# Optimization experiments

Measured on AMD Instinct MI355X. Metric: run time of the kernel, lower is better.

The kernel has to match this reference:

```python
import jax, jax.numpy as jnp
import numpy as np

N = 200000       # nodes
E = 6400000      # edges
F_IN, H1, H2, C = 7, 32, 16, 2


def gcn_conv(x, W, b, src, dst, n):
    """PyG GCNConv: add self-loops, symmetric normalization, linear, scatter-add."""
    loop = jnp.arange(n, dtype=src.dtype)
    s = jnp.concatenate([src, loop])
    d = jnp.concatenate([dst, loop])
    # degree of target nodes (with self-loops)
    deg = jax.ops.segment_sum(jnp.ones_like(d, dtype=x.dtype), d, num_segments=n)
    dinv = jnp.where(deg > 0, jax.lax.rsqrt(deg), 0.0)
    h = x @ W                                  # [n, out]
    norm = dinv[s] * dinv[d]                   # [e+n]
    msg = h[s] * norm[:, None]                 # gather + normalize
    out = jax.ops.segment_sum(msg, d, num_segments=n)  # scatter-add aggregation
    return out + b


def setup_inputs() -> dict:
    key = jax.random.key(0)
    ks = jax.random.split(key, 8)
    x = jax.random.normal(ks[0], (N, F_IN), dtype=jnp.float32)
    edge_index = jax.random.randint(ks[1], (2, E), 0, N, dtype=jnp.int64)
    def glorot(k, fan_in, fan_out):
        lim = np.sqrt(6.0 / (fan_in + fan_out)).astype(np.float32)
        return jax.random.uniform(k, (fan_in, fan_out), jnp.float32, -lim, lim)
    return {
        "x": x,
        "edge_index": edge_index,
        "W1": glorot(ks[2], F_IN, H1), "b1": jnp.zeros((H1,), jnp.float32),
        "W2": glorot(ks[3], H1, H2), "b2": jnp.zeros((H2,), jnp.float32),
        "Wfc": glorot(ks[4], H2, C), "bfc": jnp.zeros((C,), jnp.float32),
    }


def reference(x, edge_index, W1, b1, W2, b2, Wfc, bfc):
    src, dst = edge_index[0], edge_index[1]
    h = jax.nn.relu(gcn_conv(x, W1, b1, src, dst, N))
    h = jax.nn.relu(gcn_conv(h, W2, b2, src, dst, N))
    return h @ Wfc + bfc
```

## Files before the change

kernel.cpp:

```cpp
#include <hip/hip_runtime.h>

#define NNODES 200000
#define NEDGES 6400000
#define FIN 7
#define FH1 32
#define FH2 16
#define NC 2

#define WB 128
#define WB_SHIFT 7
#define NBUCK ((NNODES + WB - 1) / WB)
#define NBLK 1024
#define CHUNK (NEDGES / NBLK)
#define EPT ((CHUNK + 255) / 256)
#define PSHIFT 18
#define SRCMASK ((1u << PSHIFT) - 1)

#define RSTRIDE 4608
#define BPT ((RSTRIDE + 255) / 256)
#define SCAP 5120


__global__ __launch_bounds__(256) void zero_cnt(int* __restrict__ cnt) {
    int i = blockIdx.x * 256 + threadIdx.x;
    if (i < NBUCK) cnt[i] = 0;
}


__global__ __launch_bounds__(256) void p2_sortres(const int* __restrict__ ei,
                                                  int* __restrict__ bucket_cur,
                                                  unsigned int* __restrict__ recs) {
    __shared__ int sorted[CHUNK];
    __shared__ int lcur[NBUCK];
    __shared__ int gbase[NBUCK];
    __shared__ int sm[256];
    int t = threadIdx.x;
    int blk = blockIdx.x;

    for (int i = t; i < NBUCK; i += 256) lcur[i] = 0;
    __syncthreads();

    int ebase = blk * CHUNK;
    int es[EPT];
    int rb[EPT];
#pragma unroll
    for (int j = 0; j < EPT; ++j) {
        int idx = j * 256 + t;
        if (idx < CHUNK) {
            int e = ebase + idx;
            int src = ei[e];
            int d = ei[NEDGES + e];
            int b = d >> WB_SHIFT;
            int rank = atomicAdd(&lcur[b], 1);
            es[j] = (int)((unsigned)src | ((unsigned)(d & (WB - 1)) << PSHIFT));
            rb[j] = (b << 16) | rank;
        }
    }
    __syncthreads();

    int base7 = t * 7;
    int loc[7];
    int s = 0;
#pragma unroll
    for (int k = 0; k < 7; ++k) {
        int idx = base7 + k;
        int v = (idx < NBUCK) ? lcur[idx] : 0;
        loc[k] = v;
        s += v;
    }
    sm[t] = s;
    __syncthreads();
    for (int off = 1; off < 256; off <<= 1) {
        int v = (t >= off) ? sm[t - off] : 0;
        __syncthreads();
        sm[t] += v;
        __syncthreads();
    }
    int run = sm[t] - s;
#pragma unroll
    for (int k = 0; k < 7; ++k) {
        int idx = base7 + k;
        if (idx < NBUCK) {
            lcur[idx] = run;
            if (loc[k] > 0)
                gbase[idx] = idx * RSTRIDE + atomicAdd(&bucket_cur[idx], loc[k]);
            run += loc[k];
        }
    }
    __syncthreads();

#pragma unroll
    for (int j = 0; j < EPT; ++j) {
        int idx = j * 256 + t;
        if (idx < CHUNK) {
            int b = rb[j] >> 16;
            int rank = rb[j] & 0xffff;
            sorted[lcur[b] + rank] = es[j];
        }
    }
    __syncthreads();

    for (int i = t; i < CHUNK; i += 256) {
        int lo = 0, hi = NBUCK - 1;
        while (lo < hi) {
            int mid = (lo + hi + 1) >> 1;
            if (lcur[mid] <= i) lo = mid; else hi = mid - 1;
        }
        int b = lo;
        recs[(size_t)gbase[b] + (i - lcur[b])] = (unsigned)sorted[i];
    }
}


__global__ __launch_bounds__(256) void p2b_sort(unsigned int* __restrict__ recs,
                                                const int* __restrict__ bucket_cur,
                                                const float* __restrict__ x,
                                                int* __restrict__ node_off,
                                                float4* __restrict__ gx) {
    __shared__ int sorted[SCAP];
    __shared__ int hist[WB], st[WB];
    int t = threadIdx.x;
    int b = blockIdx.x;
    if (t < WB) hist[t] = 0;
    __syncthreads();

    int beg = b * RSTRIDE;
    int cnt = bucket_cur[b];

    int es[BPT];
    int rr[BPT];
#pragma unroll
    for (int j = 0; j < BPT; ++j) {
        int i = j * 256 + t;
        if (i < cnt) {
            unsigned r = recs[(size_t)beg + i];
            int dl = r >> PSHIFT;
            int rank = atomicAdd(&hist[dl], 1);
            es[j] = (int)(r & SRCMASK);
            rr[j] = dl | (rank << 7);
        }
    }
    __syncthreads();

    if (t < WB) st[t] = hist[t];
    __syncthreads();
    for (int off = 1; off < WB; off <<= 1) {
        int v = 0;
        if (t < WB && t >= off) v = st[t - off];
        __syncthreads();
        if (t < WB) st[t] += v;
        __syncthreads();
    }
    if (t < WB) st[t] -= hist[t];
    __syncthreads();

#pragma unroll
    for (int j = 0; j < BPT; ++j) {
        int i = j * 256 + t;
        if (i < cnt) {
            int dl = rr[j] & (WB - 1);
            int rank = rr[j] >> 7;
            sorted[st[dl] + rank] = es[j];
        }
    }
    __syncthreads();

    for (int i = t; i < cnt; i += 256)
        recs[(size_t)beg + i] = (unsigned)sorted[i];

    int node = b * WB + t;
    if (t < WB && node < NNODES) {
        node_off[node] = beg + st[t];
        float di = rsqrtf((float)(1 + hist[t]));
        const float* xr = x + (size_t)node * FIN;
        float4 v0, v1;
        v0.x = xr[0] * di; v0.y = xr[1] * di; v0.z = xr[2] * di; v0.w = xr[3] * di;
        v1.x = xr[4] * di; v1.y = xr[5] * di; v1.z = xr[6] * di; v1.w = 0.0f;
        gx[(size_t)node * 2 + 0] = v0;
        gx[(size_t)node * 2 + 1] = v1;
    }
}


__global__ __launch_bounds__(256) void l1_fast(const unsigned int* __restrict__ recs,
                                               const int* __restrict__ node_off,
                                               const int* __restrict__ bucket_cur,
                                               const float4* __restrict__ gx,
                                               const float* __restrict__ W1,
                                               const float* __restrict__ b1,
                                               const float* __restrict__ W2,
                                               float4* __restrict__ y) {
    __shared__ int sl_src[SCAP];
    __shared__ int noffs[WB + 1];
    __shared__ float acc[WB][9];
    __shared__ float sW1[FIN * FH1];
    __shared__ float sb1[FH1];
    __shared__ float sW2[FH1 * FH2];
    int t = threadIdx.x;
    for (int i = t; i < FIN * FH1; i += 256) sW1[i] = W1[i];
    if (t < FH1) sb1[t] = b1[t];
    for (int i = t; i < FH1 * FH2; i += 256) sW2[i] = W2[i];

    int b = blockIdx.x;
    int beg = b * RSTRIDE;
    int cnt_all = bucket_cur[b];
    for (int i = t; i < WB; i += 256) {
        int idx = b * WB + i;
        noffs[i] = (idx < NNODES) ? node_off[idx] : beg + cnt_all;
    }
    if (t == 0) noffs[WB] = beg + cnt_all;
    __syncthreads();

    for (int i = t; i < cnt_all; i += 256) sl_src[i] = (int)recs[(size_t)beg + i];
    __syncthreads();

    int n = t >> 1;
    int hq = t & 1;
    int base = noffs[n] - beg;
    int cnt = noffs[n + 1] - noffs[n];
    float ax = 0.0f, ay = 0.0f, az = 0.0f, aw = 0.0f;
    int k = 0;
    for (; k + 7 < cnt; k += 8) {
        int s0 = sl_src[base + k];
        int s1 = sl_src[base + k + 1];
        int s2 = sl_src[base + k + 2];
        int s3 = sl_src[base + k + 3];
        int s4 = sl_src[base + k + 4];
        int s5 = sl_src[base + k + 5];
        int s6 = sl_src[base + k + 6];
        int s7 = sl_src[base + k + 7];
        float4 v0 = gx[(size_t)s0 * 2 + hq];
        float4 v1 = gx[(size_t)s1 * 2 + hq];
        float4 v2 = gx[(size_t)s2 * 2 + hq];
        float4 v3 = gx[(size_t)s3 * 2 + hq];
        float4 v4 = gx[(size_t)s4 * 2 + hq];
        float4 v5 = gx[(size_t)s5 * 2 + hq];
        float4 v6 = gx[(size_t)s6 * 2 + hq];
        float4 v7 = gx[(size_t)s7 * 2 + hq];
        ax += v0.x + v1.x; ay += v0.y + v1.y;
        az += v0.z + v1.z; aw += v0.w + v1.w;
        ax += v2.x + v3.x; ay += v2.y + v3.y;
        az += v2.z + v3.z; aw += v2.w + v3.w;
        ax += v4.x + v5.x; ay += v4.y + v5.y;
        az += v4.z + v5.z; aw += v4.w + v5.w;
        ax += v6.x + v7.x; ay += v6.y + v7.y;
        az += v6.z + v7.z; aw += v6.w + v7.w;
    }
    for (; k < cnt; ++k) {
        int s0 = sl_src[base + k];
        float4 v0 = gx[(size_t)s0 * 2 + hq];
        ax += v0.x; ay += v0.y; az += v0.z; aw += v0.w;
    }
    int kb = hq * 4;
    acc[n][kb + 0] = ax; acc[n][kb + 1] = ay;
    acc[n][kb + 2] = az; acc[n][kb + 3] = aw;
    __syncthreads();

    int node = b * WB + t;
    if (t >= WB || node >= NNODES) return;

    float di = rsqrtf((float)(1 + (noffs[t + 1] - noffs[t])));
    float4 g0 = gx[(size_t)node * 2], g1 = gx[(size_t)node * 2 + 1];
    float xa[FIN];
    xa[0] = (acc[t][0] + g0.x) * di;
    xa[1] = (acc[t][1] + g0.y) * di;
    xa[2] = (acc[t][2] + g0.z) * di;
    xa[3] = (acc[t][3] + g0.w) * di;
    xa[4] = (acc[t][4] + g1.x) * di;
    xa[5] = (acc[t][5] + g1.y) * di;
    xa[6] = (acc[t][6] + g1.z) * di;

    float h1[FH1];
#pragma unroll
    for (int j = 0; j < FH1; ++j) h1[j] = sb1[j];
#pragma unroll
    for (int f = 0; f < FIN; ++f) {
        float xv = xa[f];
#pragma unroll
        for (int j = 0; j < FH1; ++j) h1[j] = fmaf(xv, sW1[f * FH1 + j], h1[j]);
    }
#pragma unroll
    for (int j = 0; j < FH1; ++j) h1[j] = fmaxf(h1[j], 0.0f);

    float yv[FH2];
#pragma unroll
    for (int j = 0; j < FH2; ++j) yv[j] = 0.0f;
#pragma unroll
    for (int k2 = 0; k2 < FH1; ++k2) {
        float hv = h1[k2];
#pragma unroll
        for (int j = 0; j < FH2; ++j) yv[j] = fmaf(hv, sW2[k2 * FH2 + j], yv[j]);
    }

    size_t yb = (size_t)node * 4;
    float4 o;
    o.x = yv[0] * di; o.y = yv[1] * di; o.z = yv[2] * di; o.w = yv[3] * di;
    y[yb + 0] = o;
    o.x = yv[4] * di; o.y = yv[5] * di; o.z = yv[6] * di; o.w = yv[7] * di;
    y[yb + 1] = o;
    o.x = yv[8] * di; o.y = yv[9] * di; o.z = yv[10] * di; o.w = yv[11] * di;
    y[yb + 2] = o;
    o.x = yv[12] * di; o.y = yv[13] * di; o.z = yv[14] * di; o.w = yv[15] * di;
    y[yb + 3] = o;
}


__global__ __launch_bounds__(256) void l2_fast(const unsigned int* __restrict__ recs,
                                               const int* __restrict__ node_off,
                                               const int* __restrict__ bucket_cur,
                                               const float4* __restrict__ y,
                                               const float* __restrict__ b2,
                                               const float* __restrict__ Wfc,
                                               const float* __restrict__ bfc,
                                               float2* __restrict__ out) {
    __shared__ int sl_src[SCAP];
    __shared__ int noffs[WB + 1];
    __shared__ float acc[WB][17];
    __shared__ float sb2[FH2];
    __shared__ float sWfc[FH2 * NC];
    __shared__ float sbfc[NC];
    int t = threadIdx.x;
    if (t < FH2) sb2[t] = b2[t];
    if (t < FH2 * NC) sWfc[t] = Wfc[t];
    if (t < NC) sbfc[t] = bfc[t];

    int b = blockIdx.x;
    int beg = b * RSTRIDE;
    int cnt_all = bucket_cur[b];
    for (int i = t; i < WB; i += 256) {
        int idx = b * WB + i;
        noffs[i] = (idx < NNODES) ? node_off[idx] : beg + cnt_all;
    }
    if (t == 0) noffs[WB] = beg + cnt_all;
    __syncthreads();

    for (int i = t; i < cnt_all; i += 256) sl_src[i] = (int)recs[(size_t)beg + i];
    __syncthreads();

    int q = t & 3;
#pragma unroll
    for (int r = 0; r < 2; ++r) {
        int n = (t >> 2) + 64 * r;
        int base = noffs[n] - beg;
        int cnt = noffs[n + 1] - noffs[n];
        float ax = 0.0f, ay = 0.0f, az = 0.0f, aw = 0.0f;
        int k = 0;
        for (; k + 7 < cnt; k += 8) {
            int s0 = sl_src[base + k];
            int s1 = sl_src[base + k + 1];
            int s2 = sl_src[base + k + 2];
            int s3 = sl_src[base + k + 3];
            int s4 = sl_src[base + k + 4];
            int s5 = sl_src[base + k + 5];
            int s6 = sl_src[base + k + 6];
            int s7 = sl_src[base + k + 7];
            float4 v0 = y[(size_t)s0 * 4 + q];
            float4 v1 = y[(size_t)s1 * 4 + q];
            float4 v2 = y[(size_t)s2 * 4 + q];
            float4 v3 = y[(size_t)s3 * 4 + q];
            float4 v4 = y[(size_t)s4 * 4 + q];
            float4 v5 = y[(size_t)s5 * 4 + q];
            float4 v6 = y[(size_t)s6 * 4 + q];
            float4 v7 = y[(size_t)s7 * 4 + q];
            ax += v0.x + v1.x; ay += v0.y + v1.y;
            az += v0.z + v1.z; aw += v0.w + v1.w;
            ax += v2.x + v3.x; ay += v2.y + v3.y;
            az += v2.z + v3.z; aw += v2.w + v3.w;
            ax += v4.x + v5.x; ay += v4.y + v5.y;
            az += v4.z + v5.z; aw += v4.w + v5.w;
            ax += v6.x + v7.x; ay += v6.y + v7.y;
            az += v6.z + v7.z; aw += v6.w + v7.w;
        }
        for (; k < cnt; ++k) {
            int s0 = sl_src[base + k];
            float4 v0 = y[(size_t)s0 * 4 + q];
            ax += v0.x; ay += v0.y; az += v0.z; aw += v0.w;
        }
        int kb = q * 4;
        acc[n][kb + 0] = ax; acc[n][kb + 1] = ay;
        acc[n][kb + 2] = az; acc[n][kb + 3] = aw;
    }
    __syncthreads();

    int node = b * WB + t;
    if (t >= WB || node >= NNODES) return;

    float di = rsqrtf((float)(1 + (noffs[t + 1] - noffs[t])));
    size_t yb = (size_t)node * 4;
    float4 s0 = y[yb + 0], s1 = y[yb + 1], s2 = y[yb + 2], s3 = y[yb + 3];
    float self[FH2] = {s0.x, s0.y, s0.z, s0.w, s1.x, s1.y, s1.z, s1.w,
                       s2.x, s2.y, s2.z, s2.w, s3.x, s3.y, s3.z, s3.w};

    float o0 = sbfc[0], o1 = sbfc[1];
#pragma unroll
    for (int k = 0; k < FH2; ++k) {
        float h = fmaxf(fmaf(di, acc[t][k] + self[k], sb2[k]), 0.0f);
        o0 = fmaf(h, sWfc[k * NC + 0], o0);
        o1 = fmaf(h, sWfc[k * NC + 1], o1);
    }
    float2 ov; ov.x = o0; ov.y = o1;
    out[node] = ov;
}


extern "C" void kernel_launch(void* const* d_in, const int* in_sizes, int n_in,
                              void* d_out, int out_size, void* d_ws, size_t ws_size,
                              hipStream_t stream) {
    const float* x   = (const float*)d_in[0];
    const int*   ei  = (const int*)d_in[1];
    const float* W1  = (const float*)d_in[2];
    const float* b1  = (const float*)d_in[3];
    const float* W2  = (const float*)d_in[4];
    const float* b2  = (const float*)d_in[5];
    const float* Wfc = (const float*)d_in[6];
    const float* bfc = (const float*)d_in[7];
    float* out = (float*)d_out;

    char* p = (char*)d_ws;
    auto carve = [&](size_t bytes) -> char* {
        char* r = p;
        p += (bytes + 255) & ~(size_t)255;
        return r;
    };
    int*      bucket_cur = (int*)carve((size_t)NBUCK * 4);
    int*      node_off   = (int*)carve((size_t)NNODES * 4);
    float*    gx         = (float*)carve((size_t)NNODES * 8 * 4);
    float*    y          = (float*)carve((size_t)NNODES * 16 * 4);
    unsigned* recs       = (unsigned*)carve((size_t)NBUCK * RSTRIDE * 4);

    zero_cnt<<<(NBUCK + 255) / 256, 256, 0, stream>>>(bucket_cur);
    p2_sortres<<<NBLK, 256, 0, stream>>>(ei, bucket_cur, recs);
    p2b_sort<<<NBUCK, 256, 0, stream>>>(recs, bucket_cur, x, node_off, (float4*)gx);
    l1_fast<<<NBUCK, 256, 0, stream>>>(recs, node_off, bucket_cur, (const float4*)gx,
                                       W1, b1, W2, (float4*)y);
    l2_fast<<<NBUCK, 256, 0, stream>>>(recs, node_off, bucket_cur, (const float4*)y,
                                       b2, Wfc, bfc, (float2*)out);
}
```

Measured before the change: 427.8 us.

## Enlarge edge-bucketing chunks and recompute sort keys instead of holding registers

The first bucketing pass now uses 512 blocks of 512 threads, so each block handles twice as many edges. That should cut global atomics on bucket counters and lengthen the contiguous runs written per bucket. Packed source/dst records are no longer kept in registers: edges are re-read from global memory in the scatter pass to reduce register pressure. The per-bucket local sort switches to a count-then-atomic-slot scheme that re-reads the records instead of caching ranks in registers. The cost is extra global reads, and the order of edges within each node is no longer deterministic.

Result: faster. 343.2 us, median of 2 (-19.8%).

```diff
diff --git a/kernel.cpp b/kernel.cpp
--- a/kernel.cpp
+++ b/kernel.cpp
@@ -10,14 +10,14 @@
 #define WB 128
 #define WB_SHIFT 7
 #define NBUCK ((NNODES + WB - 1) / WB)
-#define NBLK 1024
+#define BT 512
+#define NBLK 512
 #define CHUNK (NEDGES / NBLK)
-#define EPT ((CHUNK + 255) / 256)
+#define EPT ((CHUNK + BT - 1) / BT)
 #define PSHIFT 18
 #define SRCMASK ((1u << PSHIFT) - 1)
 
 #define RSTRIDE 4608
-#define BPT ((RSTRIDE + 255) / 256)
 #define SCAP 5120
 
 
@@ -27,50 +27,46 @@
 }
 
 
-__global__ __launch_bounds__(256) void p2_sortres(const int* __restrict__ ei,
-                                                  int* __restrict__ bucket_cur,
-                                                  unsigned int* __restrict__ recs) {
+__global__ __launch_bounds__(BT, 4) void p2_sortres(const int* __restrict__ ei,
+                                                    int* __restrict__ bucket_cur,
+                                                    unsigned int* __restrict__ recs) {
     __shared__ int sorted[CHUNK];
     __shared__ int lcur[NBUCK];
     __shared__ int gbase[NBUCK];
-    __shared__ int sm[256];
+    __shared__ int sm[BT];
     int t = threadIdx.x;
     int blk = blockIdx.x;
 
-    for (int i = t; i < NBUCK; i += 256) lcur[i] = 0;
+    for (int i = t; i < NBUCK; i += BT) lcur[i] = 0;
     __syncthreads();
 
     int ebase = blk * CHUNK;
-    int es[EPT];
     int rb[EPT];
 #pragma unroll
     for (int j = 0; j < EPT; ++j) {
-        int idx = j * 256 + t;
+        int idx = j * BT + t;
         if (idx < CHUNK) {
-            int e = ebase + idx;
-            int src = ei[e];
-            int d = ei[NEDGES + e];
+            int d = ei[NEDGES + ebase + idx];
             int b = d >> WB_SHIFT;
             int rank = atomicAdd(&lcur[b], 1);
-            es[j] = (int)((unsigned)src | ((unsigned)(d & (WB - 1)) << PSHIFT));
-            rb[j] = (b << 16) | rank;
-        }
-    }
-    __syncthreads();
-
-    int base7 = t * 7;
-    int loc[7];
+            rb[j] = (b << 14) | rank;
+        }
+    }
+    __syncthreads();
+
+    int base4 = t * 4;
+    int loc[4];
     int s = 0;
 #pragma unroll
-    for (int k = 0; k < 7; ++k) {
-        int idx = base7 + k;
+    for (int k = 0; k < 4; ++k) {
+        int idx = base4 + k;
         int v = (idx < NBUCK) ? lcur[idx] : 0;
         loc[k] = v;
         s += v;
     }
     sm[t] = s;
     __syncthreads();
-    for (int off = 1; off < 256; off <<= 1) {
+    for (int off = 1; off < BT; off <<= 1) {
         int v = (t >= off) ? sm[t - off] : 0;
         __syncthreads();
         sm[t] += v;
@@ -78,8 +74,8 @@
     }
     int run = sm[t] - s;
 #pragma unroll
-    for (int k = 0; k < 7; ++k) {
-        int idx = base7 + k;
+    for (int k = 0; k < 4; ++k) {
+        int idx = base4 + k;
         if (idx < NBUCK) {
             lcur[idx] = run;
             if (loc[k] > 0)
@@ -91,23 +87,26 @@
 
 #pragma unroll
     for (int j = 0; j < EPT; ++j) {
-        int idx = j * 256 + t;
+        int idx = j * BT + t;
         if (idx < CHUNK) {
-            int b = rb[j] >> 16;
-            int rank = rb[j] & 0xffff;
-            sorted[lcur[b] + rank] = es[j];
-        }
-    }
-    __syncthreads();
-
-    for (int i = t; i < CHUNK; i += 256) {
+            int e = ebase + idx;
+            int src = ei[e];
+            int d = ei[NEDGES + e];
+            int b = rb[j] >> 14;
+            int rank = rb[j] & 0x3fff;
+            sorted[lcur[b] + rank] =
+                (int)((unsigned)src | ((unsigned)(d & (WB - 1)) << PSHIFT));
+        }
+    }
+    __syncthreads();
+
+    for (int i = t; i < CHUNK; i += BT) {
         int lo = 0, hi = NBUCK - 1;
         while (lo < hi) {
             int mid = (lo + hi + 1) >> 1;
             if (lcur[mid] <= i) lo = mid; else hi = mid - 1;
         }
-        int b = lo;
-        recs[(size_t)gbase[b] + (i - lcur[b])] = (unsigned)sorted[i];
+        recs[(size_t)gbase[lo] + (i - lcur[lo])] = (unsigned)sorted[i];
     }
 }
 
@@ -118,7 +117,7 @@
                                                 int* __restrict__ node_off,
                                                 float4* __restrict__ gx) {
     __shared__ int sorted[SCAP];
-    __shared__ int hist[WB], st[WB];
+    __shared__ int hist[WB], st[WB], cur[WB];
     int t = threadIdx.x;
     int b = blockIdx.x;
     if (t < WB) hist[t] = 0;
@@ -127,41 +126,29 @@
     int beg = b * RSTRIDE;
     int cnt = bucket_cur[b];
 
-    int es[BPT];
-    int rr[BPT];
-#pragma unroll
-    for (int j = 0; j < BPT; ++j) {
-        int i = j * 256 + t;
-        if (i < cnt) {
-            unsigned r = recs[(size_t)beg + i];
-            int dl = r >> PSHIFT;
-            int rank = atomicAdd(&hist[dl], 1);
-            es[j] = (int)(r & SRCMASK);
-            rr[j] = dl | (rank << 7);
-        }
-    }
-    __syncthreads();
-
-    if (t < WB) st[t] = hist[t];
+    for (int i = t; i < cnt; i += 256)
+        atomicAdd(&hist[recs[(size_t)beg + i] >> PSHIFT], 1);
+    __syncthreads();
+
+    if (t < WB) cur[t] = hist[t];
     __syncthreads();
     for (int off = 1; off < WB; off <<= 1) {
         int v = 0;
-        if (t < WB && t >= off) v = st[t - off];
+        if (t < WB && t >= off) v = cur[t - off];
         __syncthreads();
-        if (t < WB) st[t] += v;
+        if (t < WB) cur[t] += v;
         __syncthreads();
     }
-    if (t < WB) st[t] -= hist[t];
-    __syncthreads();
-
-#pragma unroll
-    for (int j = 0; j < BPT; ++j) {
-        int i = j * 256 + t;
-        if (i < cnt) {
-            int dl = rr[j] & (WB - 1);
-            int rank = rr[j] >> 7;
-            sorted[st[dl] + rank] = es[j];
-        }
+    if (t < WB) {
+        st[t] = cur[t] - hist[t];
+        cur[t] = st[t];
+    }
+    __syncthreads();
+
+    for (int i = t; i < cnt; i += 256) {
+        unsigned r = recs[(size_t)beg + i];
+        int slot = atomicAdd(&cur[r >> PSHIFT], 1);
+        sorted[slot] = (int)(r & SRCMASK);
     }
     __syncthreads();
 
@@ -429,7 +416,7 @@
     unsigned* recs       = (unsigned*)carve((size_t)NBUCK * RSTRIDE * 4);
 
     zero_cnt<<<(NBUCK + 255) / 256, 256, 0, stream>>>(bucket_cur);
-    p2_sortres<<<NBLK, 256, 0, stream>>>(ei, bucket_cur, recs);
+    p2_sortres<<<NBLK, BT, 0, stream>>>(ei, bucket_cur, recs);
     p2b_sort<<<NBUCK, 256, 0, stream>>>(recs, bucket_cur, x, node_off, (float4*)gx);
     l1_fast<<<NBUCK, 256, 0, stream>>>(recs, node_off, bucket_cur, (const float4*)gx,
                                        W1, b1, W2, (float4*)y);
```
